# Kernel tuning notes

Hardware: AMD Instinct MI355X
Metric: run time of the kernel (lower is better)

## Reference

```python
import jax, jax.numpy as jnp
import numpy as np

N, E, D_IN, D, H, NC, L = 50000, 640000, 256, 128, 8, 47, 3
DH = D // H

def layernorm(x, g, b, eps=1e-5):
    mu = x.mean(-1, keepdims=True)
    var = ((x - mu) ** 2).mean(-1, keepdims=True)
    return (x - mu) / jnp.sqrt(var + eps) * g + b

def setup_inputs() -> dict:
    key = jax.random.key(0)
    ks = jax.random.split(key, 12)
    s = lambda k, shape, fan: jax.random.normal(k, shape, jnp.float32) * (1.0 / np.sqrt(fan))
    return dict(
        X=jax.random.normal(ks[0], (N, D_IN), jnp.float32),
        edge_index=jax.random.randint(ks[1], (2, E), 0, N, dtype=jnp.int32),
        emb_w=s(ks[2], (D_IN, D), D_IN), emb_b=jnp.zeros((D,), jnp.float32),
        emb_ln_g=jnp.ones((D,), jnp.float32), emb_ln_b=jnp.zeros((D,), jnp.float32),
        Wq=s(ks[3], (L, D, D), D), Wk=s(ks[4], (L, D, D), D),
        Wv=s(ks[5], (L, D, D), D), Wo=s(ks[6], (L, D, D), D),
        ln_g=jnp.ones((L, D), jnp.float32), ln_b=jnp.zeros((L, D), jnp.float32),
        f1_w=s(ks[7], (D, 512), D), f1_b=jnp.zeros((512,), jnp.float32),
        f2_w=s(ks[8], (512, 512), 512), f2_b=jnp.zeros((512,), jnp.float32),
        f3_w=s(ks[9], (512, NC), 512), f3_b=jnp.zeros((NC,), jnp.float32),
    )

def reference(X, edge_index, emb_w, emb_b, emb_ln_g, emb_ln_b, Wq, Wk, Wv, Wo, ln_g, ln_b, f1_w, f1_b, f2_w, f2_b, f3_w, f3_b):
    # embedding: Linear -> ReLU -> LayerNorm
    h = layernorm(jax.nn.relu(X @ emb_w + emb_b), emb_ln_g, emb_ln_b)  # [N, D]
    src, dst = edge_index[0], edge_index[1]
    scale = 1.0 / np.sqrt(DH)
    for l in range(L):  # small fixed layer loop
        q = (h @ Wq[l]).reshape(N, H, DH)
        k = (h @ Wk[l]).reshape(N, H, DH)
        v = (h @ Wv[l]).reshape(N, H, DH)
        # per-edge attention scores, softmax over incoming edges of each dst node
        scores = jnp.einsum('ehd,ehd->eh', q[dst], k[src]) * scale  # [E, H]
        m = jax.ops.segment_max(scores, dst, num_segments=N)        # [N, H]
        a = jnp.exp(scores - m[dst])
        denom = jax.ops.segment_sum(a, dst, num_segments=N)         # [N, H]
        a = a / denom[dst]
        msg = a[..., None] * v[src]                                  # [E, H, DH]
        agg = jax.ops.segment_sum(msg, dst, num_segments=N).reshape(N, D)
        h = layernorm(h + agg @ Wo[l], ln_g[l], ln_b[l])
    # feed_forward head
    h = jax.nn.relu(h @ f1_w + f1_b)
    h = jax.nn.relu(h @ f2_w + f2_b)
    return h @ f3_w + f3_b  # [N, NC]
```

## Files before the change

### kernel.cpp

```cpp
#include <hip/hip_runtime.h>
#include <hip/hip_bf16.h>
#include <math.h>


typedef __bf16 bf16x8 __attribute__((ext_vector_type(8)));
typedef __bf16 bf16x4 __attribute__((ext_vector_type(4)));
typedef float  f32x4  __attribute__((ext_vector_type(4)));

#define MFMA16(a, b, c) __builtin_amdgcn_mfma_f32_16x16x32_bf16((a), (b), (c), 0, 0, 0)

__device__ __forceinline__ void ld_lds16(const __bf16* g, __bf16* l) {
    __builtin_amdgcn_global_load_lds(
        (__attribute__((address_space(1))) void*)g,
        (__attribute__((address_space(3))) void*)l, 16, 0, 0);
}


__global__ __launch_bounds__(256) void zero_ints(int* __restrict__ p, int n) {
    int i = blockIdx.x * 256 + threadIdx.x;
    if (i < n) p[i] = 0;
}

__global__ __launch_bounds__(256) void count_deg(const int* __restrict__ ei,
                                                 int* __restrict__ deg, int E) {
    int e = blockIdx.x * 256 + threadIdx.x;
    if (e < E) atomicAdd(&deg[ei[(size_t)E + e]], 1);
}

__global__ __launch_bounds__(256) void scan_part(const int* __restrict__ deg,
                                                 int* __restrict__ partials, int N) {
    int b = blockIdx.x, t = threadIdx.x, lane = t & 63, w = t >> 6;
    int base = b * 1024 + t * 4;
    int4 v = make_int4(0, 0, 0, 0);
    if (base + 3 < N) v = *(const int4*)&deg[base];
    else {
        if (base < N)     v.x = deg[base];
        if (base + 1 < N) v.y = deg[base + 1];
        if (base + 2 < N) v.z = deg[base + 2];
    }
    int s = v.x + v.y + v.z + v.w;
#pragma unroll
    for (int o = 1; o < 64; o <<= 1) s += __shfl_xor(s, o);
    __shared__ int ws[4];
    if (lane == 0) ws[w] = s;
    __syncthreads();
    if (t == 0) partials[b] = ws[0] + ws[1] + ws[2] + ws[3];
}

__global__ __launch_bounds__(64) void scan_mid(int* __restrict__ partials,
                                               int* __restrict__ row_ptr,
                                               int nb, int N) {
    int t = threadIdx.x;
    int v = (t < nb) ? partials[t] : 0;
    int incl = v;
#pragma unroll
    for (int o = 1; o < 64; o <<= 1) {
        int u = __shfl_up(incl, o);
        if (t >= o) incl += u;
    }
    if (t < nb) partials[t] = incl - v;
    if (t == nb - 1) row_ptr[N] = incl;
}

__global__ __launch_bounds__(256) void scan_final(const int* __restrict__ deg,
                                                  const int* __restrict__ partials,
                                                  int* __restrict__ row_ptr, int N) {
    int b = blockIdx.x, t = threadIdx.x, lane = t & 63, w = t >> 6;
    int base = b * 1024 + t * 4;
    int4 v = make_int4(0, 0, 0, 0);
    if (base + 3 < N) v = *(const int4*)&deg[base];
    else {
        if (base < N)     v.x = deg[base];
        if (base + 1 < N) v.y = deg[base + 1];
        if (base + 2 < N) v.z = deg[base + 2];
    }
    int c1 = v.x, c2 = c1 + v.y, c3 = c2 + v.z, c4 = c3 + v.w;
    int s = c4, incl = s;
#pragma unroll
    for (int o = 1; o < 64; o <<= 1) {
        int u = __shfl_up(incl, o);
        if (lane >= o) incl += u;
    }
    int texcl = incl - s;
    __shared__ int ws[4];
    if (lane == 63) ws[w] = incl;
    __syncthreads();
    int woff = 0;
    for (int i = 0; i < w; ++i) woff += ws[i];
    int off = partials[b] + woff + texcl;
    if (base < N)     row_ptr[base]     = off;
    if (base + 1 < N) row_ptr[base + 1] = off + c1;
    if (base + 2 < N) row_ptr[base + 2] = off + c2;
    if (base + 3 < N) row_ptr[base + 3] = off + c3;
}

__global__ __launch_bounds__(256) void scatter_edges(const int* __restrict__ ei,
                                                     const int* __restrict__ row_ptr,
                                                     int* __restrict__ cursor,
                                                     int* __restrict__ csr_src, int E) {
    int e = blockIdx.x * 256 + threadIdx.x;
    if (e < E) {
        int d = ei[(size_t)E + e];
        int pos = row_ptr[d] + atomicAdd(&cursor[d], 1);
        csr_src[pos] = ei[e];
    }
}


__global__ __launch_bounds__(256) void transpose_all(
    const float* __restrict__ emb_w, const float* __restrict__ f1w,
    const float* __restrict__ f2w, const float* __restrict__ f3w,
    const float* __restrict__ Wq, const float* __restrict__ Wk,
    const float* __restrict__ Wv, const float* __restrict__ Wo,
    __bf16* __restrict__ embT, __bf16* __restrict__ f1T,
    __bf16* __restrict__ f2T, __bf16* __restrict__ f3T,
    __bf16* __restrict__ qkvT, __bf16* __restrict__ woT) {
    __shared__ float tile[32][33];
    int t = blockIdx.x;
    const float* src; __bf16* dst; int K, Nin, Npad, nxt;
    if (t < 32)       { src = emb_w; dst = embT; K = 256; Nin = 128; Npad = 128; nxt = 4; }
    else if (t < 96)  { t -= 32;  src = f1w; dst = f1T; K = 128; Nin = 512; Npad = 512; nxt = 16; }
    else if (t < 352) { t -= 96;  src = f2w; dst = f2T; K = 512; Nin = 512; Npad = 512; nxt = 16; }
    else if (t < 384) { t -= 352; src = f3w; dst = f3T; K = 512; Nin = 47;  Npad = 48;  nxt = 2; }
    else {
        t -= 384;
        int mat = t >> 4; t &= 15;
        int l = mat >> 2, m = mat & 3;
        src = (m == 0 ? Wq : m == 1 ? Wk : m == 2 ? Wv : Wo) + (size_t)l * 16384;
        dst = (m < 3) ? qkvT + (size_t)l * 49152 + (size_t)m * 16384
                      : woT + (size_t)l * 16384;
        K = 128; Nin = 128; Npad = 128; nxt = 4;
    }
    int n0 = (t % nxt) * 32, k0 = (t / nxt) * 32;
    int tx = threadIdx.x & 31, ty = threadIdx.x >> 5;
#pragma unroll
    for (int i = 0; i < 32; i += 8) {
        int k = k0 + ty + i, n = n0 + tx;
        tile[ty + i][tx] = (k < K && n < Nin) ? src[(size_t)k * Nin + n] : 0.f;
    }
    __syncthreads();
#pragma unroll
    for (int i = 0; i < 32; i += 8) {
        int n = n0 + ty + i, k = k0 + tx;
        if (n < Npad && k < K) dst[(size_t)n * K + k] = (__bf16)tile[tx][ty + i];
    }
}


template <int NK, int EPI>
__global__ __launch_bounds__(256) void gemm_tile(const __bf16* __restrict__ A,
                                                 const __bf16* __restrict__ BT,
                                                 const float* __restrict__ bias,
                                                 void* __restrict__ Cv,
                                                 int M, int ldc, int ncols) {
    constexpr int K = NK * 32;
    __shared__ __bf16 As[2][4096];
    __shared__ __bf16 Bs[2][4096];
    int t = threadIdx.x, w = t >> 6, lane = t & 63;
    int cb = lane & 15, rq = (lane >> 4) * 4;
    int n0 = blockIdx.x * 128, m0 = blockIdx.y * 128;

    int sr = lane & 15;
    int sk = (lane >> 4) * 8;
    int ar0 = m0 + (2 * w) * 16 + sr;     if (ar0 >= M) ar0 = M - 1;
    int ar1 = m0 + (2 * w + 1) * 16 + sr; if (ar1 >= M) ar1 = M - 1;
    const __bf16* ag0 = A + (size_t)ar0 * K + sk;
    const __bf16* ag1 = A + (size_t)ar1 * K + sk;
    const __bf16* bg0 = BT + (size_t)(n0 + (2 * w) * 16 + sr) * K + sk;
    const __bf16* bg1 = BT + (size_t)(n0 + (2 * w + 1) * 16 + sr) * K + sk;
    __bf16* la0[2] = { &As[0][(2 * w) * 512],     &As[1][(2 * w) * 512] };
    __bf16* la1[2] = { &As[0][(2 * w + 1) * 512], &As[1][(2 * w + 1) * 512] };
    __bf16* lb0[2] = { &Bs[0][(2 * w) * 512],     &Bs[1][(2 * w) * 512] };
    __bf16* lb1[2] = { &Bs[0][(2 * w + 1) * 512], &Bs[1][(2 * w + 1) * 512] };

    ld_lds16(ag0, la0[0]);
    ld_lds16(ag1, la1[0]);
    ld_lds16(bg0, lb0[0]);
    ld_lds16(bg1, lb1[0]);
    __syncthreads();

    int wm = w >> 1, wn = w & 1;
    f32x4 acc[4][4];
#pragma unroll
    for (int i = 0; i < 4; ++i)
#pragma unroll
        for (int j = 0; j < 4; ++j) acc[i][j] = (f32x4){0.f, 0.f, 0.f, 0.f};

#pragma unroll
    for (int ks = 0; ks < NK; ++ks) {
        int cur = ks & 1;
        if (ks + 1 < NK) {
            int nxt = cur ^ 1;
            ld_lds16(ag0 + (ks + 1) * 32, la0[nxt]);
            ld_lds16(ag1 + (ks + 1) * 32, la1[nxt]);
            ld_lds16(bg0 + (ks + 1) * 32, lb0[nxt]);
            ld_lds16(bg1 + (ks + 1) * 32, lb1[nxt]);
        }
        bf16x8 af[4], bfr[4];
#pragma unroll
        for (int i = 0; i < 4; ++i)
            af[i] = *(const bf16x8*)&As[cur][(wm * 4 + i) * 512 + lane * 8];
#pragma unroll
        for (int j = 0; j < 4; ++j)
            bfr[j] = *(const bf16x8*)&Bs[cur][(wn * 4 + j) * 512 + lane * 8];
#pragma unroll
        for (int j = 0; j < 4; ++j)
#pragma unroll
            for (int i = 0; i < 4; ++i)
                acc[i][j] = MFMA16(af[i], bfr[j], acc[i][j]);
        __syncthreads();
    }

#pragma unroll
    for (int j = 0; j < 4; ++j) {
        int col = n0 + (wn * 4 + j) * 16 + cb;
        float bb = 0.f;
        if (EPI >= 1 && col < ncols) bb = bias[col];
#pragma unroll
        for (int i = 0; i < 4; ++i) {
#pragma unroll
            for (int ii = 0; ii < 4; ++ii) {
                int row = m0 + (wm * 4 + i) * 16 + rq + ii;
                if (row >= M) continue;
                float v = acc[i][j][ii] + bb;
                if (EPI == 0) {
                    ((__bf16*)Cv)[(size_t)row * ldc + col] = (__bf16)v;
                } else if (EPI == 1) {
                    ((__bf16*)Cv)[(size_t)row * ldc + col] = (__bf16)fmaxf(v, 0.f);
                } else {
                    if (col < ncols)
                        ((float*)Cv)[(size_t)row * ldc + col] = v;
                }
            }
        }
    }
}


template <int K, bool EMB>
__global__ __launch_bounds__(64) void gemm_ln(const void* __restrict__ Av,
                                              const __bf16* __restrict__ BT,
                                              const float* __restrict__ bias,
                                              const float* resid,
                                              const float* __restrict__ g,
                                              const float* __restrict__ beta,
                                              float* hout, __bf16* __restrict__ hbf,
                                              int M) {
    int wid = blockIdx.x;
    int lane = threadIdx.x;
    int m0 = wid * 16;
    if (m0 >= M) return;
    constexpr int KS = K / 32;
    int cb = lane & 15;
    int kc = (lane >> 4) * 8;
    int rq = (lane >> 4) * 4;
    int arow = m0 + cb;
    if (arow >= M) arow = M - 1;

    bf16x8 a[KS];
    if constexpr (EMB) {
        const float* A = (const float*)Av;
#pragma unroll
        for (int ks = 0; ks < KS; ++ks) {
            float4 u0 = *(const float4*)&A[(size_t)arow * K + ks * 32 + kc];
            float4 u1 = *(const float4*)&A[(size_t)arow * K + ks * 32 + kc + 4];
            bf16x8 av;
            av[0] = (__bf16)u0.x; av[1] = (__bf16)u0.y; av[2] = (__bf16)u0.z; av[3] = (__bf16)u0.w;
            av[4] = (__bf16)u1.x; av[5] = (__bf16)u1.y; av[6] = (__bf16)u1.z; av[7] = (__bf16)u1.w;
            a[ks] = av;
        }
    } else {
        const __bf16* A = (const __bf16*)Av;
#pragma unroll
        for (int ks = 0; ks < KS; ++ks)
            a[ks] = *(const bf16x8*)&A[(size_t)arow * K + ks * 32 + kc];
    }

    const __bf16* bbase = &BT[(size_t)cb * K + kc];
    bf16x8 bA[KS], bB[KS];
#pragma unroll
    for (int ks = 0; ks < KS; ++ks) bA[ks] = *(const bf16x8*)(bbase + ks * 32);

    f32x4 acc[8];
#pragma unroll
    for (int nt = 0; nt < 8; ++nt) acc[nt] = (f32x4){0.f, 0.f, 0.f, 0.f};

#pragma unroll
    for (int nt = 0; nt < 8; nt += 2) {
#pragma unroll
        for (int ks = 0; ks < KS; ++ks)
            bB[ks] = *(const bf16x8*)(bbase + (size_t)(nt + 1) * 16 * K + ks * 32);
#pragma unroll
        for (int ks = 0; ks < KS; ++ks)
            acc[nt] = MFMA16(a[ks], bA[ks], acc[nt]);
        if (nt + 2 < 8) {
#pragma unroll
            for (int ks = 0; ks < KS; ++ks)
                bA[ks] = *(const bf16x8*)(bbase + (size_t)(nt + 2) * 16 * K + ks * 32);
        }
#pragma unroll
        for (int ks = 0; ks < KS; ++ks)
            acc[nt + 1] = MFMA16(a[ks], bB[ks], acc[nt + 1]);
    }

#pragma unroll
    for (int nt = 0; nt < 8; ++nt) {
        int col = nt * 16 + cb;
        float bb = EMB ? bias[col] : 0.f;
#pragma unroll
        for (int i = 0; i < 4; ++i) {
            float v = acc[nt][i];
            if (EMB) {
                v = fmaxf(v + bb, 0.f);
            } else {
                int row = m0 + rq + i;
                if (row >= M) row = M - 1;
                v += resid[(size_t)row * 128 + col];
            }
            acc[nt][i] = v;
        }
    }

    float s[4] = {0.f, 0.f, 0.f, 0.f}, qs[4] = {0.f, 0.f, 0.f, 0.f};
#pragma unroll
    for (int nt = 0; nt < 8; ++nt)
#pragma unroll
        for (int i = 0; i < 4; ++i) {
            float v = acc[nt][i];
            s[i] += v;
            qs[i] += v * v;
        }
#pragma unroll
    for (int i = 0; i < 4; ++i)
#pragma unroll
        for (int o = 1; o < 16; o <<= 1) {
            s[i] += __shfl_xor(s[i], o);
            qs[i] += __shfl_xor(qs[i], o);
        }
    float mu[4], rstd[4];
#pragma unroll
    for (int i = 0; i < 4; ++i) {
        mu[i] = s[i] * (1.f / 128.f);
        float var = qs[i] * (1.f / 128.f) - mu[i] * mu[i];
        rstd[i] = rsqrtf(var + 1e-5f);
    }

#pragma unroll
    for (int nt = 0; nt < 8; ++nt) {
        int col = nt * 16 + cb;
        float gv = g[col], bv = beta[col];
#pragma unroll
        for (int i = 0; i < 4; ++i) {
            int row = m0 + rq + i;
            if (row >= M) continue;
            float y = (acc[nt][i] - mu[i]) * rstd[i] * gv + bv;
            size_t idx = (size_t)row * 128 + col;
            hout[idx] = y;
            hbf[idx] = (__bf16)y;
        }
    }
}


__global__ __launch_bounds__(256) void attn_gat(const __bf16* __restrict__ qkv,
                                                const int* __restrict__ row_ptr,
                                                const int* __restrict__ csr_src,
                                                __bf16* __restrict__ agg, int N) {
    int wave = threadIdx.x >> 6;
    int lane = threadIdx.x & 63;
    int n = blockIdx.x * 4 + wave;
    if (n >= N) return;
    int j = lane >> 4, q16 = lane & 15, c0 = q16 * 8;
    const float scale = 0.25f;

    bf16x8 qv = *(const bf16x8*)&qkv[(size_t)n * 384 + c0];
    float qf[8];
#pragma unroll
    for (int i = 0; i < 8; ++i) qf[i] = (float)qv[i];

    int e0 = row_ptr[n], e1 = row_ptr[n + 1];
    float m = -3e38f, s = 0.f;
    float acc[8] = {0.f, 0.f, 0.f, 0.f, 0.f, 0.f, 0.f, 0.f};

    for (int base = e0; base < e1; base += 4) {
        int e = base + j;
        bool valid = e < e1;
        int src = csr_src[valid ? e : e0];
        const __bf16* kp = &qkv[(size_t)src * 384 + 128 + c0];
        bf16x8 kv = *(const bf16x8*)kp;
        bf16x8 vv = *(const bf16x8*)(kp + 128);
        float d = 0.f;
#pragma unroll
        for (int i = 0; i < 8; ++i) d = fmaf(qf[i], (float)kv[i], d);
        d += __shfl_xor(d, 1);
        float sc = d * scale;
        if (valid) {
            float mn = fmaxf(m, sc);
            float f = __expf(m - mn), p = __expf(sc - mn);
            s = s * f + p;
#pragma unroll
            for (int i = 0; i < 8; ++i) acc[i] = acc[i] * f + p * (float)vv[i];
            m = mn;
        }
    }

#pragma unroll
    for (int off = 16; off <= 32; off <<= 1) {
        float mo_ = __shfl_xor(m, off);
        float so_ = __shfl_xor(s, off);
        float mn = fmaxf(m, mo_);
        float f = __expf(m - mn), fo = __expf(mo_ - mn);
        s = s * f + so_ * fo;
#pragma unroll
        for (int i = 0; i < 8; ++i)
            acc[i] = acc[i] * f + __shfl_xor(acc[i], off) * fo;
        m = mn;
    }

    if (j == 0) {
        float inv = (s > 0.f) ? 1.f / s : 0.f;
        bf16x8 o;
#pragma unroll
        for (int i = 0; i < 8; ++i) o[i] = (__bf16)(acc[i] * inv);
        *(bf16x8*)&agg[(size_t)n * 128 + c0] = o;
    }
}


__global__ __launch_bounds__(512) void ffn_mfma(const __bf16* __restrict__ hbf,
                                                const __bf16* __restrict__ f1T,
                                                const float* __restrict__ f1b,
                                                const __bf16* __restrict__ f2T,
                                                const float* __restrict__ f2b,
                                                const __bf16* __restrict__ f3T,
                                                const float* __restrict__ f3b,
                                                float* __restrict__ out, int M) {
    __shared__ __bf16 hbuf[64 * 512];
    int w = threadIdx.x >> 6;
    int lane = threadIdx.x & 63;
    int r0 = blockIdx.x * 64;
    int cb = lane & 15;
    int kc = (lane >> 4) * 8;
    int rq = (lane >> 4) * 4;
    char* hb = (char*)hbuf;

    {
        bf16x8 a1[4][4];
#pragma unroll
        for (int mt = 0; mt < 4; ++mt) {
            int row = r0 + mt * 16 + cb;
            if (row >= M) row = M - 1;
#pragma unroll
            for (int ks = 0; ks < 4; ++ks)
                a1[mt][ks] = *(const bf16x8*)&hbf[(size_t)row * 128 + ks * 32 + kc];
        }
        const __bf16* b1base = &f1T[(size_t)(w * 64 + cb) * 128 + kc];
        bf16x8 bA[4], bB[4];
#pragma unroll
        for (int ks = 0; ks < 4; ++ks) bA[ks] = *(const bf16x8*)(b1base + ks * 32);
#pragma unroll
        for (int nt = 0; nt < 4; nt += 2) {
#pragma unroll
            for (int ks = 0; ks < 4; ++ks)
                bB[ks] = *(const bf16x8*)(b1base + (size_t)(nt + 1) * 16 * 128 + ks * 32);
            {
                f32x4 acc[4];
#pragma unroll
                for (int mt = 0; mt < 4; ++mt) acc[mt] = (f32x4){0.f, 0.f, 0.f, 0.f};
#pragma unroll
                for (int ks = 0; ks < 4; ++ks)
#pragma unroll
                    for (int mt = 0; mt < 4; ++mt)
                        acc[mt] = MFMA16(a1[mt][ks], bA[ks], acc[mt]);
                int ncol = w * 64 + nt * 16;
                float bb = f1b[ncol + cb];
#pragma unroll
                for (int mt = 0; mt < 4; ++mt)
#pragma unroll
                    for (int i = 0; i < 4; ++i) {
                        int rl = mt * 16 + rq + i;
                        int byte = (rl * 1024 + (ncol + cb) * 2) ^ ((rl & 7) << 4);
                        *(__bf16*)(hb + byte) = (__bf16)fmaxf(acc[mt][i] + bb, 0.f);
                    }
            }
            if (nt + 2 < 4) {
#pragma unroll
                for (int ks = 0; ks < 4; ++ks)
                    bA[ks] = *(const bf16x8*)(b1base + (size_t)(nt + 2) * 16 * 128 + ks * 32);
            }
            {
                f32x4 acc[4];
#pragma unroll
                for (int mt = 0; mt < 4; ++mt) acc[mt] = (f32x4){0.f, 0.f, 0.f, 0.f};
#pragma unroll
                for (int ks = 0; ks < 4; ++ks)
#pragma unroll
                    for (int mt = 0; mt < 4; ++mt)
                        acc[mt] = MFMA16(a1[mt][ks], bB[ks], acc[mt]);
                int ncol = w * 64 + (nt + 1) * 16;
                float bb = f1b[ncol + cb];
#pragma unroll
                for (int mt = 0; mt < 4; ++mt)
#pragma unroll
                    for (int i = 0; i < 4; ++i) {
                        int rl = mt * 16 + rq + i;
                        int byte = (rl * 1024 + (ncol + cb) * 2) ^ ((rl & 7) << 4);
                        *(__bf16*)(hb + byte) = (__bf16)fmaxf(acc[mt][i] + bb, 0.f);
                    }
            }
        }
    }
    __syncthreads();

    {
        f32x4 acc2[4][4];
#pragma unroll
        for (int mt = 0; mt < 4; ++mt)
#pragma unroll
            for (int nt = 0; nt < 4; ++nt) acc2[mt][nt] = (f32x4){0.f, 0.f, 0.f, 0.f};

        const __bf16* bp[4];
#pragma unroll
        for (int nt = 0; nt < 4; ++nt)
            bp[nt] = &f2T[(size_t)(w * 64 + nt * 16 + cb) * 512 + kc];

        bf16x8 b0[4], b1[4];
#pragma unroll
        for (int nt = 0; nt < 4; ++nt) b0[nt] = *(const bf16x8*)bp[nt];

#pragma unroll
        for (int ks = 0; ks < 16; ks += 2) {
#pragma unroll
            for (int nt = 0; nt < 4; ++nt)
                b1[nt] = *(const bf16x8*)(bp[nt] + (ks + 1) * 32);
            {
                bf16x8 a2[4];
#pragma unroll
                for (int mt = 0; mt < 4; ++mt) {
                    int rl = mt * 16 + cb;
                    int byte = (rl * 1024 + (ks * 32 + kc) * 2) ^ ((rl & 7) << 4);
                    a2[mt] = *(const bf16x8*)(hb + byte);
                }
#pragma unroll
                for (int nt = 0; nt < 4; ++nt)
#pragma unroll
                    for (int mt = 0; mt < 4; ++mt)
                        acc2[mt][nt] = MFMA16(a2[mt], b0[nt], acc2[mt][nt]);
            }
            if (ks + 2 < 16) {
#pragma unroll
                for (int nt = 0; nt < 4; ++nt)
                    b0[nt] = *(const bf16x8*)(bp[nt] + (ks + 2) * 32);
            }
            {
                bf16x8 a2[4];
#pragma unroll
                for (int mt = 0; mt < 4; ++mt) {
                    int rl = mt * 16 + cb;
                    int byte = (rl * 1024 + ((ks + 1) * 32 + kc) * 2) ^ ((rl & 7) << 4);
                    a2[mt] = *(const bf16x8*)(hb + byte);
                }
#pragma unroll
                for (int nt = 0; nt < 4; ++nt)
#pragma unroll
                    for (int mt = 0; mt < 4; ++mt)
                        acc2[mt][nt] = MFMA16(a2[mt], b1[nt], acc2[mt][nt]);
            }
        }
        __syncthreads();

#pragma unroll
        for (int nt = 0; nt < 4; ++nt) {
            int ncol = w * 64 + nt * 16;
            float bb = f2b[ncol + cb];
#pragma unroll
            for (int mt = 0; mt < 4; ++mt)
#pragma unroll
                for (int i = 0; i < 4; ++i) {
                    int rl = mt * 16 + rq + i;
                    int byte = (rl * 1024 + (ncol + cb) * 2) ^ ((rl & 7) << 4);
                    *(__bf16*)(hb + byte) = (__bf16)fmaxf(acc2[mt][nt][i] + bb, 0.f);
                }
        }
    }
    __syncthreads();

    if (w < 4) {
        f32x4 acc3[3];
#pragma unroll
        for (int nt = 0; nt < 3; ++nt) acc3[nt] = (f32x4){0.f, 0.f, 0.f, 0.f};
        const __bf16* b3base = &f3T[(size_t)cb * 512 + kc];
#pragma unroll
        for (int ks = 0; ks < 16; ++ks) {
            int rl = w * 16 + cb;
            int byte = (rl * 1024 + (ks * 32 + kc) * 2) ^ ((rl & 7) << 4);
            bf16x8 a3 = *(const bf16x8*)(hb + byte);
#pragma unroll
            for (int nt = 0; nt < 3; ++nt) {
                bf16x8 b = *(const bf16x8*)(b3base + (size_t)nt * 16 * 512 + ks * 32);
                acc3[nt] = MFMA16(a3, b, acc3[nt]);
            }
        }
#pragma unroll
        for (int nt = 0; nt < 3; ++nt) {
            int col = nt * 16 + cb;
            if (col < 47) {
                float bb = f3b[col];
                int r = r0 + w * 16 + rq;
#pragma unroll
                for (int i = 0; i < 4; ++i)
                    if (r + i < M) out[(size_t)(r + i) * 47 + col] = acc3[nt][i] + bb;
            }
        }
    }
}


extern "C" void kernel_launch(void* const* d_in, const int* in_sizes, int n_in,
                              void* d_out, int out_size, void* d_ws, size_t ws_size,
                              hipStream_t stream) {
    const float* X        = (const float*)d_in[0];
    const int*   ei       = (const int*)d_in[1];
    const float* emb_w    = (const float*)d_in[2];
    const float* emb_b    = (const float*)d_in[3];
    const float* emb_ln_g = (const float*)d_in[4];
    const float* emb_ln_b = (const float*)d_in[5];
    const float* Wq       = (const float*)d_in[6];
    const float* Wk       = (const float*)d_in[7];
    const float* Wv       = (const float*)d_in[8];
    const float* Wo       = (const float*)d_in[9];
    const float* ln_g     = (const float*)d_in[10];
    const float* ln_b     = (const float*)d_in[11];
    const float* f1w      = (const float*)d_in[12];
    const float* f1b      = (const float*)d_in[13];
    const float* f2w      = (const float*)d_in[14];
    const float* f2b      = (const float*)d_in[15];
    const float* f3w      = (const float*)d_in[16];
    const float* f3b      = (const float*)d_in[17];

    const int N = in_sizes[0] / 256;
    const int E = in_sizes[1] / 2;
    const int NB = (N + 1023) / 1024;

    char* p = (char*)d_ws;
    float* h = (float*)p;            p += (size_t)N * 128 * 4;
    __bf16* hbf = (__bf16*)p;        p += (size_t)N * 128 * 2;
    __bf16* qkv = (__bf16*)p;        p += (size_t)N * 384 * 2;
    __bf16* aggb = (__bf16*)p;       p += (size_t)N * 128 * 2;
    __bf16* embT = (__bf16*)p;       p += 128 * 256 * 2;
    __bf16* qkvT = (__bf16*)p;       p += 3 * 384 * 128 * 2;
    __bf16* woT = (__bf16*)p;        p += 3 * 128 * 128 * 2;
    __bf16* f1T = (__bf16*)p;        p += 512 * 128 * 2;
    __bf16* f2T = (__bf16*)p;        p += 512 * 512 * 2;
    __bf16* f3T = (__bf16*)p;        p += 48 * 512 * 2;
    int* deg = (int*)p;              p += (size_t)N * 4;
    int* cursor = (int*)p;           p += (size_t)N * 4;
    int* row_ptr = (int*)p;          p += (size_t)(N + 1) * 4;
    int* csr_src = (int*)p;          p += (size_t)E * 4;
    int* partials = (int*)p;

    zero_ints<<<(2 * N + 255) / 256, 256, 0, stream>>>(deg, 2 * N);
    count_deg<<<(E + 255) / 256, 256, 0, stream>>>(ei, deg, E);
    scan_part<<<NB, 256, 0, stream>>>(deg, partials, N);
    scan_mid<<<1, 64, 0, stream>>>(partials, row_ptr, NB, N);
    scan_final<<<NB, 256, 0, stream>>>(deg, partials, row_ptr, N);
    scatter_edges<<<(E + 255) / 256, 256, 0, stream>>>(ei, row_ptr, cursor, csr_src, E);

    transpose_all<<<576, 256, 0, stream>>>(emb_w, f1w, f2w, f3w, Wq, Wk, Wv, Wo,
                                           embT, f1T, f2T, f3T, qkvT, woT);

    int gwave = (N + 15) / 16;
    int gm128 = (N + 127) / 128;

    gemm_ln<256, true><<<gwave, 64, 0, stream>>>(X, embT, emb_b, nullptr,
                                                 emb_ln_g, emb_ln_b, h, hbf, N);

    for (int l = 0; l < 3; ++l) {
        gemm_tile<4, 0><<<dim3(3, gm128), 256, 0, stream>>>(
            hbf, qkvT + (size_t)l * 49152, nullptr, qkv, N, 384, 384);
        attn_gat<<<(N + 3) / 4, 256, 0, stream>>>(qkv, row_ptr, csr_src, aggb, N);
        gemm_ln<128, false><<<gwave, 64, 0, stream>>>(aggb, woT + (size_t)l * 16384,
                                                      nullptr, h,
                                                      ln_g + (size_t)l * 128,
                                                      ln_b + (size_t)l * 128, h, hbf, N);
    }

    ffn_mfma<<<(N + 63) / 64, 512, 0, stream>>>(hbf, f1T, f1b, f2T, f2b, f3T, f3b,
                                                (float*)d_out, N);
}
```

Baseline: 544.5 us.

## Prefetch next-edge gathers in attention, pre-pack FFN weight fragments, memset degrees

The attention kernel now software-pipelines its edge loop: it loads the next group's K/V rows and the index after that while the current group's scores and online softmax are computed, so gather latency overlaps with compute. A new pack_frag kernel rearranges the transposed FFN weights into MFMA fragment order, making each wave's B-operand loads contiguous 1 KB chunks instead of strided rows. The zero_ints kernel is replaced by hipMemsetAsync. The costs are more live registers in attn_gat, one extra small launch, and a second copy of the FFN weights in the workspace.

```diff
diff --git a/kernel.cpp b/kernel.cpp
--- a/kernel.cpp
+++ b/kernel.cpp
@@ -4,7 +4,6 @@
 
 
 typedef __bf16 bf16x8 __attribute__((ext_vector_type(8)));
-typedef __bf16 bf16x4 __attribute__((ext_vector_type(4)));
 typedef float  f32x4  __attribute__((ext_vector_type(4)));
 
 #define MFMA16(a, b, c) __builtin_amdgcn_mfma_f32_16x16x32_bf16((a), (b), (c), 0, 0, 0)
@@ -15,11 +14,6 @@
         (__attribute__((address_space(3))) void*)l, 16, 0, 0);
 }
 
-
-__global__ __launch_bounds__(256) void zero_ints(int* __restrict__ p, int n) {
-    int i = blockIdx.x * 256 + threadIdx.x;
-    if (i < n) p[i] = 0;
-}
 
 __global__ __launch_bounds__(256) void count_deg(const int* __restrict__ ei,
                                                  int* __restrict__ deg, int E) {
@@ -147,6 +141,28 @@
 }
 
 
+__global__ __launch_bounds__(256) void pack_frag(const __bf16* __restrict__ f1T,
+                                                 const __bf16* __restrict__ f2T,
+                                                 const __bf16* __restrict__ f3T,
+                                                 __bf16* __restrict__ f1P,
+                                                 __bf16* __restrict__ f2P,
+                                                 __bf16* __restrict__ f3P) {
+    int idx = blockIdx.x * 256 + threadIdx.x;
+    const __bf16* src; __bf16* dst; int K, base;
+    if (idx < 8192)        { src = f1T; dst = f1P; K = 128; base = idx; }
+    else if (idx < 40960)  { src = f2T; dst = f2P; K = 512; base = idx - 8192; }
+    else if (idx < 44032)  { src = f3T; dst = f3P; K = 512; base = idx - 40960; }
+    else return;
+    int lane = base & 63;
+    int nks = K / 32;
+    int ks = (base >> 6) % nks;
+    int tile = base / (64 * nks);
+    int cb = lane & 15, kcg = lane >> 4;
+    bf16x8 v = *(const bf16x8*)&src[(size_t)(tile * 16 + cb) * K + ks * 32 + kcg * 8];
+    *(bf16x8*)&dst[(size_t)base * 8] = v;
+}
+
+
 template <int NK, int EPI>
 __global__ __launch_bounds__(256) void gemm_tile(const __bf16* __restrict__ A,
                                                  const __bf16* __restrict__ BT,
@@ -373,34 +389,53 @@
     int j = lane >> 4, q16 = lane & 15, c0 = q16 * 8;
     const float scale = 0.25f;
 
+    int e0 = row_ptr[n], e1 = row_ptr[n + 1];
+
     bf16x8 qv = *(const bf16x8*)&qkv[(size_t)n * 384 + c0];
     float qf[8];
 #pragma unroll
     for (int i = 0; i < 8; ++i) qf[i] = (float)qv[i];
 
-    int e0 = row_ptr[n], e1 = row_ptr[n + 1];
     float m = -3e38f, s = 0.f;
     float acc[8] = {0.f, 0.f, 0.f, 0.f, 0.f, 0.f, 0.f, 0.f};
 
-    for (int base = e0; base < e1; base += 4) {
-        int e = base + j;
-        bool valid = e < e1;
-        int src = csr_src[valid ? e : e0];
-        const __bf16* kp = &qkv[(size_t)src * 384 + 128 + c0];
-        bf16x8 kv = *(const bf16x8*)kp;
-        bf16x8 vv = *(const bf16x8*)(kp + 128);
-        float d = 0.f;
-#pragma unroll
-        for (int i = 0; i < 8; ++i) d = fmaf(qf[i], (float)kv[i], d);
-        d += __shfl_xor(d, 1);
-        float sc = d * scale;
-        if (valid) {
-            float mn = fmaxf(m, sc);
-            float f = __expf(m - mn), p = __expf(sc - mn);
-            s = s * f + p;
-#pragma unroll
-            for (int i = 0; i < 8; ++i) acc[i] = acc[i] * f + p * (float)vv[i];
-            m = mn;
+    if (e0 < e1) {
+        int e = e0 + j;
+        bool v0 = e < e1;
+        int i0 = csr_src[v0 ? e : e0];
+        const __bf16* kp0 = &qkv[(size_t)i0 * 384 + 128 + c0];
+        bf16x8 k0 = *(const bf16x8*)kp0;
+        bf16x8 vv0 = *(const bf16x8*)(kp0 + 128);
+        int en = e0 + 4 + j;
+        bool v1 = en < e1;
+        int i1 = csr_src[v1 ? en : e0];
+
+        for (int base = e0; base < e1; base += 4) {
+            bf16x8 k1, vv1;
+            if (base + 4 < e1) {
+                const __bf16* kp1 = &qkv[(size_t)i1 * 384 + 128 + c0];
+                k1 = *(const bf16x8*)kp1;
+                vv1 = *(const bf16x8*)(kp1 + 128);
+            }
+            int e2 = base + 8 + j;
+            bool v2 = e2 < e1;
+            int i2 = csr_src[v2 ? e2 : e0];
+
+            float d = 0.f;
+#pragma unroll
+            for (int i = 0; i < 8; ++i) d = fmaf(qf[i], (float)k0[i], d);
+            d += __shfl_xor(d, 1);
+            float sc = d * scale;
+            if (v0) {
+                float mn = fmaxf(m, sc);
+                float f = __expf(m - mn), p = __expf(sc - mn);
+                s = s * f + p;
+#pragma unroll
+                for (int i = 0; i < 8; ++i) acc[i] = acc[i] * f + p * (float)vv0[i];
+                m = mn;
+            }
+            k0 = k1; vv0 = vv1; v0 = v1;
+            i1 = i2; v1 = v2;
         }
     }
 
@@ -428,11 +463,11 @@
 
 
 __global__ __launch_bounds__(512) void ffn_mfma(const __bf16* __restrict__ hbf,
-                                                const __bf16* __restrict__ f1T,
+                                                const __bf16* __restrict__ f1P,
                                                 const float* __restrict__ f1b,
-                                                const __bf16* __restrict__ f2T,
+                                                const __bf16* __restrict__ f2P,
                                                 const float* __restrict__ f2b,
-                                                const __bf16* __restrict__ f3T,
+                                                const __bf16* __restrict__ f3P,
                                                 const float* __restrict__ f3b,
                                                 float* __restrict__ out, int M) {
     __shared__ __bf16 hbuf[64 * 512];
@@ -454,15 +489,15 @@
             for (int ks = 0; ks < 4; ++ks)
                 a1[mt][ks] = *(const bf16x8*)&hbf[(size_t)row * 128 + ks * 32 + kc];
         }
-        const __bf16* b1base = &f1T[(size_t)(w * 64 + cb) * 128 + kc];
+        const __bf16* b1p = f1P + (size_t)(w * 4) * 4 * 512 + lane * 8;
         bf16x8 bA[4], bB[4];
 #pragma unroll
-        for (int ks = 0; ks < 4; ++ks) bA[ks] = *(const bf16x8*)(b1base + ks * 32);
+        for (int ks = 0; ks < 4; ++ks) bA[ks] = *(const bf16x8*)(b1p + ks * 512);
 #pragma unroll
         for (int nt = 0; nt < 4; nt += 2) {
 #pragma unroll
             for (int ks = 0; ks < 4; ++ks)
-                bB[ks] = *(const bf16x8*)(b1base + (size_t)(nt + 1) * 16 * 128 + ks * 32);
+                bB[ks] = *(const bf16x8*)(b1p + ((nt + 1) * 4 + ks) * 512);
             {
                 f32x4 acc[4];
 #pragma unroll
@@ -486,7 +521,7 @@
             if (nt + 2 < 4) {
 #pragma unroll
                 for (int ks = 0; ks < 4; ++ks)
-                    bA[ks] = *(const bf16x8*)(b1base + (size_t)(nt + 2) * 16 * 128 + ks * 32);
+                    bA[ks] = *(const bf16x8*)(b1p + ((nt + 2) * 4 + ks) * 512);
             }
             {
                 f32x4 acc[4];
@@ -519,20 +554,17 @@
 #pragma unroll
             for (int nt = 0; nt < 4; ++nt) acc2[mt][nt] = (f32x4){0.f, 0.f, 0.f, 0.f};
 
-        const __bf16* bp[4];
-#pragma unroll
-        for (int nt = 0; nt < 4; ++nt)
-            bp[nt] = &f2T[(size_t)(w * 64 + nt * 16 + cb) * 512 + kc];
+        const __bf16* b2p = f2P + (size_t)(w * 4) * 16 * 512 + lane * 8;
 
         bf16x8 b0[4], b1[4];
 #pragma unroll
-        for (int nt = 0; nt < 4; ++nt) b0[nt] = *(const bf16x8*)bp[nt];
+        for (int nt = 0; nt < 4; ++nt) b0[nt] = *(const bf16x8*)(b2p + nt * 16 * 512);
 
 #pragma unroll
         for (int ks = 0; ks < 16; ks += 2) {
 #pragma unroll
             for (int nt = 0; nt < 4; ++nt)
-                b1[nt] = *(const bf16x8*)(bp[nt] + (ks + 1) * 32);
+                b1[nt] = *(const bf16x8*)(b2p + (nt * 16 + ks + 1) * 512);
             {
                 bf16x8 a2[4];
 #pragma unroll
@@ -550,7 +582,7 @@
             if (ks + 2 < 16) {
 #pragma unroll
                 for (int nt = 0; nt < 4; ++nt)
-                    b0[nt] = *(const bf16x8*)(bp[nt] + (ks + 2) * 32);
+                    b0[nt] = *(const bf16x8*)(b2p + (nt * 16 + ks + 2) * 512);
             }
             {
                 bf16x8 a2[4];
@@ -589,7 +621,7 @@
         f32x4 acc3[3];
 #pragma unroll
         for (int nt = 0; nt < 3; ++nt) acc3[nt] = (f32x4){0.f, 0.f, 0.f, 0.f};
-        const __bf16* b3base = &f3T[(size_t)cb * 512 + kc];
+        const __bf16* b3p = f3P + lane * 8;
 #pragma unroll
         for (int ks = 0; ks < 16; ++ks) {
             int rl = w * 16 + cb;
@@ -597,7 +629,7 @@
             bf16x8 a3 = *(const bf16x8*)(hb + byte);
 #pragma unroll
             for (int nt = 0; nt < 3; ++nt) {
-                bf16x8 b = *(const bf16x8*)(b3base + (size_t)nt * 16 * 512 + ks * 32);
+                bf16x8 b = *(const bf16x8*)(b3p + (nt * 16 + ks) * 512);
                 acc3[nt] = MFMA16(a3, b, acc3[nt]);
             }
         }
@@ -653,13 +685,16 @@
     __bf16* f1T = (__bf16*)p;        p += 512 * 128 * 2;
     __bf16* f2T = (__bf16*)p;        p += 512 * 512 * 2;
     __bf16* f3T = (__bf16*)p;        p += 48 * 512 * 2;
+    __bf16* f1P = (__bf16*)p;        p += 8192 * 8 * 2;
+    __bf16* f2P = (__bf16*)p;        p += 32768 * 8 * 2;
+    __bf16* f3P = (__bf16*)p;        p += 3072 * 8 * 2;
     int* deg = (int*)p;              p += (size_t)N * 4;
     int* cursor = (int*)p;           p += (size_t)N * 4;
     int* row_ptr = (int*)p;          p += (size_t)(N + 1) * 4;
     int* csr_src = (int*)p;          p += (size_t)E * 4;
     int* partials = (int*)p;
 
-    zero_ints<<<(2 * N + 255) / 256, 256, 0, stream>>>(deg, 2 * N);
+    hipMemsetAsync(deg, 0, (size_t)2 * N * 4, stream);
     count_deg<<<(E + 255) / 256, 256, 0, stream>>>(ei, deg, E);
     scan_part<<<NB, 256, 0, stream>>>(deg, partials, N);
     scan_mid<<<1, 64, 0, stream>>>(partials, row_ptr, NB, N);
@@ -668,6 +703,7 @@
 
     transpose_all<<<576, 256, 0, stream>>>(emb_w, f1w, f2w, f3w, Wq, Wk, Wv, Wo,
                                            embT, f1T, f2T, f3T, qkvT, woT);
+    pack_frag<<<172, 256, 0, stream>>>(f1T, f2T, f3T, f1P, f2P, f3P);
 
     int gwave = (N + 15) / 16;
     int gm128 = (N + 127) / 128;
@@ -685,6 +721,6 @@
                                                       ln_b + (size_t)l * 128, h, hbf, N);
     }
 
-    ffn_mfma<<<(N + 63) / 64, 512, 0, stream>>>(hbf, f1T, f1b, f2T, f2b, f3T, f3b,
+    ffn_mfma<<<(N + 63) / 64, 512, 0, stream>>>(hbf, f1P, f1b, f2P, f2b, f3P, f3b,
                                                 (float*)d_out, N);
 }
```

After: 492.6 us. 1.11x faster.
